# Optimization experiments

Measured on AMD Instinct MI355X. Metric: run time of the kernel, lower is better.

The kernel has to match this reference:

```python
import jax, jax.numpy as jnp
import numpy as np

N_NODES = 50000
E_RAW = 1600000
EMB_DIM = 32
HID = 128
OUT = 128


def setup_inputs() -> dict:
    key = jax.random.key(0)
    k1, k2, k3, k4, k5, k6 = jax.random.split(key, 6)
    x = jnp.arange(N_NODES, dtype=jnp.int64)
    edge_index = jax.random.randint(k1, (2, E_RAW), 0, N_NODES, dtype=jnp.int64)
    emb = jax.random.normal(k2, (N_NODES, EMB_DIM), dtype=jnp.float32)
    W1 = jax.random.normal(k3, (EMB_DIM, HID), dtype=jnp.float32) / np.sqrt(EMB_DIM)
    b1 = jnp.zeros((HID,), dtype=jnp.float32)
    W2 = jax.random.normal(k4, (HID, OUT), dtype=jnp.float32) / np.sqrt(HID)
    b2 = jnp.zeros((OUT,), dtype=jnp.float32)
    return {"x": x, "edge_index": edge_index, "emb": emb,
            "W1": W1, "b1": b1, "W2": W2, "b2": b2}


def _gcn_norm(edge_index, num_nodes):
    # add self-loops, then symmetric normalization deg^-1/2 A_hat deg^-1/2
    loop = jnp.arange(num_nodes, dtype=edge_index.dtype)
    src = jnp.concatenate([edge_index[0], loop])
    dst = jnp.concatenate([edge_index[1], loop])
    ones = jnp.ones(src.shape[0], dtype=jnp.float32)
    deg = jax.ops.segment_sum(ones, dst, num_segments=num_nodes)
    dinv = jax.lax.rsqrt(deg)  # deg >= 1 due to self-loops
    norm = dinv[src] * dinv[dst]  # [E+N]
    return src, dst, norm


def _gcn_conv(h, src, dst, norm, W, b, num_nodes):
    h = h @ W                                  # [N, d_out] dense GEMM
    msg = h[src] * norm[:, None]               # gather + edge scale
    agg = jax.ops.segment_sum(msg, dst, num_segments=num_nodes)  # scatter-add
    return agg + b


def reference(x, edge_index, emb, W1, b1, W2, b2):
    num_nodes = emb.shape[0]
    h = emb[x]                                 # embedding lookup
    src, dst, norm = _gcn_norm(edge_index, num_nodes)
    h = _gcn_conv(h, src, dst, norm, W1, b1, num_nodes)
    h = jax.nn.relu(h)
    out = _gcn_conv(h, src, dst, norm, W2, b2, num_nodes)
    return out
```

## Files before the change

kernel.cpp:

```cpp
#include <hip/hip_runtime.h>


#define NPP   6250
#define NC    32

static inline int cdiv(int a, int b){ return (a + b - 1) / b; }

__device__ __forceinline__ unsigned short f2bf(float f){
    unsigned int u = __float_as_uint(f);
    u += 0x7fffu + ((u >> 16) & 1u);
    return (unsigned short)(u >> 16);
}
__device__ __forceinline__ float bf2f(unsigned short b){
    return __uint_as_float(((unsigned int)b) << 16);
}

__global__ void k_zero_i32(int* __restrict__ p, int n){
    int i = blockIdx.x * blockDim.x + threadIdx.x;
    if (i < n) p[i] = 0;
}

__global__ __launch_bounds__(256) void k_bucket(const int* __restrict__ src,
        const int* __restrict__ dst, int E, int* __restrict__ staged,
        int* __restrict__ gcur, int npp, int C){
    __shared__ int qcnt[8];
    __shared__ int qbase[8];
    __shared__ int qbuf[8 * 256];
    int tid = threadIdx.x;
    if (tid < 8) qcnt[tid] = 0;
    __syncthreads();
    int e0 = blockIdx.x * 1024 + tid * 4;
    if (e0 + 3 < E){
        int4 d4 = *(const int4*)(dst + e0);
        int4 s4 = *(const int4*)(src + e0);
        int dd[4] = {d4.x, d4.y, d4.z, d4.w};
        int ss[4] = {s4.x, s4.y, s4.z, s4.w};
        #pragma unroll
        for (int i = 0; i < 4; i++){
            int p = dd[i] / npp;
            int pk = ((dd[i] - p * npp) << 17) | ss[i];
            int pos = atomicAdd(&qcnt[p], 1);
            if (pos < 256) qbuf[p * 256 + pos] = pk;
            else {
                int gp = atomicAdd(&gcur[p], 1);
                staged[(size_t)p * C + gp] = pk;
            }
        }
    } else {
        for (int e = e0; e < E && e < e0 + 4; e++){
            int d = dst[e], s = src[e];
            int p = d / npp;
            int pk = ((d - p * npp) << 17) | s;
            int pos = atomicAdd(&qcnt[p], 1);
            if (pos < 256) qbuf[p * 256 + pos] = pk;
            else {
                int gp = atomicAdd(&gcur[p], 1);
                staged[(size_t)p * C + gp] = pk;
            }
        }
    }
    __syncthreads();
    if (tid < 8){
        int nq = min(qcnt[tid], 256);
        qbase[tid] = (nq > 0) ? atomicAdd(&gcur[tid], nq) : 0;
    }
    __syncthreads();
    for (int b = 0; b < 8; b++){
        int nq = min(qcnt[b], 256);
        int gb = qbase[b];
        for (int i = tid; i < nq; i += 256)
            staged[(size_t)b * C + gb + i] = qbuf[b * 256 + i];
    }
}

__global__ __launch_bounds__(256) void k_hist(const int* __restrict__ staged,
        const int* __restrict__ gcur, int C, int CH, int npp,
        unsigned short* __restrict__ H){
    __shared__ int hist[NPP];
    int part  = blockIdx.x & 7;
    int chunk = blockIdx.x >> 3;
    int tid = threadIdx.x;
    for (int i = tid; i < npp; i += 256) hist[i] = 0;
    __syncthreads();
    int pc = gcur[part];
    int e0 = chunk * CH, e1 = min(e0 + CH, pc);
    const int* sd = staged + (size_t)part * C;
    for (int e = e0 + tid; e < e1; e += 256)
        atomicAdd(&hist[(unsigned)sd[e] >> 17], 1);
    __syncthreads();
    unsigned short* Hrow = H + (size_t)(part * NC + chunk) * npp;
    for (int i = tid; i < npp; i += 256) Hrow[i] = (unsigned short)hist[i];
}

__global__ __launch_bounds__(256) void k_nodescan(unsigned short* __restrict__ H,
        int npp, int n, int* __restrict__ ecount, float* __restrict__ dinv,
        int* __restrict__ bsum){
    __shared__ int s[256];
    int t = blockIdx.x * 256 + threadIdx.x;
    int run = 0;
    if (t < 8 * npp && t < n){
        int p  = t / npp;
        int dl = t - p * npp;
        #pragma unroll
        for (int c = 0; c < NC; c++){
            size_t idx = (size_t)(p * NC + c) * npp + dl;
            int v = H[idx];
            H[idx] = (unsigned short)run;
            run += v;
        }
        ecount[t] = run;
        dinv[t] = rsqrtf((float)run + 1.0f);
    }
    s[threadIdx.x] = run;
    __syncthreads();
    for (int d = 128; d > 0; d >>= 1){
        if (threadIdx.x < d) s[threadIdx.x] += s[threadIdx.x + d];
        __syncthreads();
    }
    if (threadIdx.x == 0) bsum[blockIdx.x] = s[0];
}

__global__ __launch_bounds__(256) void k_scanBC(const int* __restrict__ ecount, int n,
        const int* __restrict__ bsum, int nb, int* __restrict__ offsets){
    __shared__ int bs[256];
    __shared__ int s[256];
    int t = threadIdx.x;
    bs[t] = (t < nb) ? bsum[t] : 0;
    __syncthreads();
    if (t == 0){
        int run = 0;
        for (int b = 0; b < nb; b++){ int v = bs[b]; bs[b] = run; run += v; }
    }
    __syncthreads();
    int i = blockIdx.x * 256 + t;
    int v = (i < n) ? ecount[i] : 0;
    s[t] = v;
    __syncthreads();
    for (int d = 1; d < 256; d <<= 1){
        int x = (t >= d) ? s[t - d] : 0;
        __syncthreads();
        s[t] += x;
        __syncthreads();
    }
    if (i < n) offsets[i] = bs[blockIdx.x] + s[t] - v;
}

__global__ __launch_bounds__(256) void k_fill3(const int* __restrict__ staged,
        const int* __restrict__ gcur, int C, int CH, int npp,
        const unsigned short* __restrict__ H, const int* __restrict__ offsets,
        int* __restrict__ csr_src){
    __shared__ int cur[NPP];
    int part  = blockIdx.x & 7;
    int chunk = blockIdx.x >> 3;
    int tid = threadIdx.x;
    const unsigned short* Hrow = H + (size_t)(part * NC + chunk) * npp;
    for (int i = tid; i < npp; i += 256) cur[i] = Hrow[i];
    __syncthreads();
    int pc = gcur[part];
    int lo = part * npp;
    int e0 = chunk * CH, e1 = min(e0 + CH, pc);
    const int* sd = staged + (size_t)part * C;
    for (int e = e0 + tid; e < e1; e += 256){
        int pk = sd[e];
        int dl = (unsigned)pk >> 17;
        int r = atomicAdd(&cur[dl], 1);
        csr_src[offsets[lo + dl] + r] = pk & 0x1FFFF;
    }
}

__global__ void k_scale(const float* __restrict__ emb, const int* __restrict__ x,
                        const float* __restrict__ dinv, unsigned short* __restrict__ es, int n){
    int idx = blockIdx.x * blockDim.x + threadIdx.x;
    if (idx >= n * 8) return;
    int i  = idx >> 3;
    int c4 = (idx & 7) * 4;
    float dv = dinv[i];
    float4 v = *(const float4*)(emb + (size_t)x[i] * 32 + c4);
    ushort4 o;
    o.x = f2bf(v.x * dv); o.y = f2bf(v.y * dv);
    o.z = f2bf(v.z * dv); o.w = f2bf(v.w * dv);
    *(ushort4*)(es + (size_t)i * 32 + c4) = o;
}

__global__ __launch_bounds__(256) void k_l1(const unsigned short* __restrict__ es,
        const int* __restrict__ offsets, const int* __restrict__ ecount,
        const int* __restrict__ csr, const float* __restrict__ dinv,
        const float* __restrict__ W1, const float* __restrict__ b1,
        unsigned short* __restrict__ hs, int n){
    __shared__ float w[32 * 128];
    __shared__ float a1t[8][32];
    for (int i = threadIdx.x; i < 32 * 128; i += 256) w[i] = W1[i];
    int g    = threadIdx.x >> 5;
    int lane = threadIdx.x & 31;
    int node = blockIdx.x * 8 + g;
    if (node < n){
        int off = offsets[node], cnt = ecount[node];
        float s0 = bf2f(es[(size_t)node * 32 + lane]);
        float s1 = 0.f;
        int e = 0;
        for (; e + 16 <= cnt; e += 16){
            int idx[16];
            #pragma unroll
            for (int i = 0; i < 16; i++) idx[i] = csr[off + e + i];
            unsigned short v[16];
            #pragma unroll
            for (int i = 0; i < 16; i++) v[i] = es[(size_t)idx[i] * 32 + lane];
            #pragma unroll
            for (int i = 0; i < 16; i += 2){
                s0 += bf2f(v[i]);
                s1 += bf2f(v[i + 1]);
            }
        }
        for (; e + 8 <= cnt; e += 8){
            int idx[8];
            #pragma unroll
            for (int i = 0; i < 8; i++) idx[i] = csr[off + e + i];
            unsigned short v[8];
            #pragma unroll
            for (int i = 0; i < 8; i++) v[i] = es[(size_t)idx[i] * 32 + lane];
            #pragma unroll
            for (int i = 0; i < 8; i += 2){
                s0 += bf2f(v[i]);
                s1 += bf2f(v[i + 1]);
            }
        }
        for (; e < cnt; e++) s0 += bf2f(es[(size_t)csr[off + e] * 32 + lane]);
        a1t[g][lane] = dinv[node] * (s0 + s1);
    }
    __syncthreads();
    if (node >= n) return;
    int c4 = lane * 4;
    float4 acc = *(const float4*)(b1 + c4);
    #pragma unroll
    for (int k4 = 0; k4 < 8; k4++){
        float4 av = *(const float4*)&a1t[g][k4 * 4];
        float4 w0 = *(const float4*)&w[(k4 * 4 + 0) * 128 + c4];
        float4 w1 = *(const float4*)&w[(k4 * 4 + 1) * 128 + c4];
        float4 w2 = *(const float4*)&w[(k4 * 4 + 2) * 128 + c4];
        float4 w3 = *(const float4*)&w[(k4 * 4 + 3) * 128 + c4];
        acc.x += av.x * w0.x + av.y * w1.x + av.z * w2.x + av.w * w3.x;
        acc.y += av.x * w0.y + av.y * w1.y + av.z * w2.y + av.w * w3.y;
        acc.z += av.x * w0.z + av.y * w1.z + av.z * w2.z + av.w * w3.z;
        acc.w += av.x * w0.w + av.y * w1.w + av.z * w2.w + av.w * w3.w;
    }
    float dv = dinv[node];
    ushort4 o;
    o.x = f2bf(dv * fmaxf(acc.x, 0.f));
    o.y = f2bf(dv * fmaxf(acc.y, 0.f));
    o.z = f2bf(dv * fmaxf(acc.z, 0.f));
    o.w = f2bf(dv * fmaxf(acc.w, 0.f));
    *(ushort4*)(hs + (size_t)node * 128 + c4) = o;
}

__global__ __launch_bounds__(256) void k_l2(const unsigned short* __restrict__ hs,
        const int* __restrict__ offsets, const int* __restrict__ ecount,
        const int* __restrict__ csr, const float* __restrict__ dinv,
        const float* __restrict__ W2, const float* __restrict__ b2,
        float* __restrict__ out, int n){
    __shared__ float a2t[32 * 128];
    int g    = threadIdx.x >> 5;
    int lane = threadIdx.x & 31;
    int c4g  = lane * 4;
    #pragma unroll
    for (int j = 0; j < 4; j++){
        int nl = g + 8 * j;
        int node = blockIdx.x * 32 + nl;
        if (node < n){
            int off = offsets[node], cnt = ecount[node];
            ushort4 sv = *(const ushort4*)(hs + (size_t)node * 128 + c4g);
            float ax0 = bf2f(sv.x), ax1 = 0.f;
            float ay0 = bf2f(sv.y), ay1 = 0.f;
            float az0 = bf2f(sv.z), az1 = 0.f;
            float aw0 = bf2f(sv.w), aw1 = 0.f;
            int e = 0;
            for (; e + 8 <= cnt; e += 8){
                int i0 = csr[off + e + 0], i1 = csr[off + e + 1];
                int i2 = csr[off + e + 2], i3 = csr[off + e + 3];
                int i4 = csr[off + e + 4], i5 = csr[off + e + 5];
                int i6 = csr[off + e + 6], i7 = csr[off + e + 7];
                ushort4 v0 = *(const ushort4*)(hs + (size_t)i0 * 128 + c4g);
                ushort4 v1 = *(const ushort4*)(hs + (size_t)i1 * 128 + c4g);
                ushort4 v2 = *(const ushort4*)(hs + (size_t)i2 * 128 + c4g);
                ushort4 v3 = *(const ushort4*)(hs + (size_t)i3 * 128 + c4g);
                ushort4 v4 = *(const ushort4*)(hs + (size_t)i4 * 128 + c4g);
                ushort4 v5 = *(const ushort4*)(hs + (size_t)i5 * 128 + c4g);
                ushort4 v6 = *(const ushort4*)(hs + (size_t)i6 * 128 + c4g);
                ushort4 v7 = *(const ushort4*)(hs + (size_t)i7 * 128 + c4g);
                ax0 += bf2f(v0.x) + bf2f(v2.x) + bf2f(v4.x) + bf2f(v6.x);
                ax1 += bf2f(v1.x) + bf2f(v3.x) + bf2f(v5.x) + bf2f(v7.x);
                ay0 += bf2f(v0.y) + bf2f(v2.y) + bf2f(v4.y) + bf2f(v6.y);
                ay1 += bf2f(v1.y) + bf2f(v3.y) + bf2f(v5.y) + bf2f(v7.y);
                az0 += bf2f(v0.z) + bf2f(v2.z) + bf2f(v4.z) + bf2f(v6.z);
                az1 += bf2f(v1.z) + bf2f(v3.z) + bf2f(v5.z) + bf2f(v7.z);
                aw0 += bf2f(v0.w) + bf2f(v2.w) + bf2f(v4.w) + bf2f(v6.w);
                aw1 += bf2f(v1.w) + bf2f(v3.w) + bf2f(v5.w) + bf2f(v7.w);
            }
            for (; e < cnt; e++){
                ushort4 v = *(const ushort4*)(hs + (size_t)csr[off + e] * 128 + c4g);
                ax0 += bf2f(v.x); ay0 += bf2f(v.y); az0 += bf2f(v.z); aw0 += bf2f(v.w);
            }
            float dv = dinv[node];
            float4 r;
            r.x = dv * (ax0 + ax1); r.y = dv * (ay0 + ay1);
            r.z = dv * (az0 + az1); r.w = dv * (aw0 + aw1);
            *(float4*)&a2t[nl * 128 + c4g] = r;
        }
    }
    __syncthreads();
    int c4 = lane * 4;
    int r0 = (threadIdx.x >> 5) * 4;
    float4 bias = *(const float4*)(b2 + c4);
    float4 acc0 = bias, acc1 = bias, acc2 = bias, acc3 = bias;
    for (int k = 0; k < 128; k += 4){
        float4 a0  = *(const float4*)&a2t[(r0 + 0) * 128 + k];
        float4 a1v = *(const float4*)&a2t[(r0 + 1) * 128 + k];
        float4 a2v = *(const float4*)&a2t[(r0 + 2) * 128 + k];
        float4 a3v = *(const float4*)&a2t[(r0 + 3) * 128 + k];
        #pragma unroll
        for (int kk = 0; kk < 4; kk++){
            float4 wv = *(const float4*)(W2 + (size_t)(k + kk) * 128 + c4);
            float b0 = (kk == 0) ? a0.x  : (kk == 1) ? a0.y  : (kk == 2) ? a0.z  : a0.w;
            float b1v= (kk == 0) ? a1v.x : (kk == 1) ? a1v.y : (kk == 2) ? a1v.z : a1v.w;
            float b2v= (kk == 0) ? a2v.x : (kk == 1) ? a2v.y : (kk == 2) ? a2v.z : a2v.w;
            float b3 = (kk == 0) ? a3v.x : (kk == 1) ? a3v.y : (kk == 2) ? a3v.z : a3v.w;
            acc0.x += b0 * wv.x; acc0.y += b0 * wv.y; acc0.z += b0 * wv.z; acc0.w += b0 * wv.w;
            acc1.x += b1v * wv.x; acc1.y += b1v * wv.y; acc1.z += b1v * wv.z; acc1.w += b1v * wv.w;
            acc2.x += b2v * wv.x; acc2.y += b2v * wv.y; acc2.z += b2v * wv.z; acc2.w += b2v * wv.w;
            acc3.x += b3 * wv.x; acc3.y += b3 * wv.y; acc3.z += b3 * wv.z; acc3.w += b3 * wv.w;
        }
    }
    int rb = blockIdx.x * 32 + r0;
    if (rb + 0 < n) *(float4*)(out + (size_t)(rb + 0) * 128 + c4) = acc0;
    if (rb + 1 < n) *(float4*)(out + (size_t)(rb + 1) * 128 + c4) = acc1;
    if (rb + 2 < n) *(float4*)(out + (size_t)(rb + 2) * 128 + c4) = acc2;
    if (rb + 3 < n) *(float4*)(out + (size_t)(rb + 3) * 128 + c4) = acc3;
}

extern "C" void kernel_launch(void* const* d_in, const int* in_sizes, int n_in,
                              void* d_out, int out_size, void* d_ws, size_t ws_size,
                              hipStream_t stream){
    const int*   x    = (const int*)d_in[0];
    const int*   ei   = (const int*)d_in[1];
    const float* emb  = (const float*)d_in[2];
    const float* W1   = (const float*)d_in[3];
    const float* b1   = (const float*)d_in[4];
    const float* W2   = (const float*)d_in[5];
    const float* b2   = (const float*)d_in[6];
    const int N = in_sizes[0];
    const int E = in_sizes[1] / 2;
    const int* srcv = ei;
    const int* dstv = ei + E;
    float* out = (float*)d_out;

    char* p = (char*)d_ws;
    auto alloc = [&](size_t bytes) -> char* {
        char* r = p; p += (bytes + 255) & ~(size_t)255; return r;
    };
    int nb = cdiv(N, 256);
    int*            ecount  = (int*)           alloc((size_t)(N + 8) * 4);
    int*            gcur    = ecount + N;
    int*            offsets = (int*)           alloc((size_t)N * 4);
    int*            bsum    = (int*)           alloc((size_t)nb * 4);
    float*          dinv    = (float*)         alloc((size_t)N * 4);
    int*            csr     = (int*)           alloc((size_t)E * 4);
    unsigned short* es      = (unsigned short*)alloc((size_t)N * 32 * 2);
    unsigned short* H       = (unsigned short*)alloc((size_t)8 * NC * NPP * 2);
    unsigned short* hs      = (unsigned short*)alloc((size_t)N * 128 * 2);
    int*            staged  = (int*)           alloc((size_t)(E + 8 * 65536) * 4);
    (void)ws_size; (void)n_in; (void)out_size;

    const int npp = cdiv(N, 8);
    const int C   = E / 8 + 65536;
    const int CH  = cdiv(C, NC);

    k_zero_i32<<<1, 64, 0, stream>>>(gcur, 8);
    k_bucket  <<<cdiv(E, 1024), 256, 0, stream>>>(srcv, dstv, E, staged, gcur, npp, C);
    k_hist    <<<8 * NC, 256, 0, stream>>>(staged, gcur, C, CH, npp, H);
    k_nodescan<<<nb, 256, 0, stream>>>(H, npp, N, ecount, dinv, bsum);
    k_scanBC  <<<nb, 256, 0, stream>>>(ecount, N, bsum, nb, offsets);
    k_fill3   <<<8 * NC, 256, 0, stream>>>(staged, gcur, C, CH, npp, H, offsets, csr);

    k_scale <<<cdiv(N * 8, 256), 256, 0, stream>>>(emb, x, dinv, es, N);
    k_l1    <<<cdiv(N, 8), 256, 0, stream>>>(es, offsets, ecount, csr, dinv, W1, b1, hs, N);

    k_l2    <<<cdiv(N, 32), 256, 0, stream>>>(hs, offsets, ecount, csr, dinv, W2, b2, out, N);
}
```

Measured before the change: 266.6 us.

## Software-pipeline layer-2 gather over two interleaved nodes per warp group

The layer-2 aggregation now handles two destination nodes at once. It software-pipelines the CSR index loads and the bf16 row gathers, prefetching the next batch of 8 indices and rows while accumulating the current batch. This raises memory-level parallelism to hide gather latency in the edge-sum loop. It also adds a launch-bounds minimum of 5 blocks, which costs extra registers for the prefetch buffers and risks spills under the tighter register cap.

```diff
diff --git a/kernel.cpp b/kernel.cpp
--- a/kernel.cpp
+++ b/kernel.cpp
@@ -13,6 +13,41 @@
 }
 __device__ __forceinline__ float bf2f(unsigned short b){
     return __uint_as_float(((unsigned int)b) << 16);
+}
+
+#define ACC8(a, v) do { \
+    a[0] += bf2f(v[0].x) + bf2f(v[2].x) + bf2f(v[4].x) + bf2f(v[6].x); \
+    a[1] += bf2f(v[1].x) + bf2f(v[3].x) + bf2f(v[5].x) + bf2f(v[7].x); \
+    a[2] += bf2f(v[0].y) + bf2f(v[2].y) + bf2f(v[4].y) + bf2f(v[6].y); \
+    a[3] += bf2f(v[1].y) + bf2f(v[3].y) + bf2f(v[5].y) + bf2f(v[7].y); \
+    a[4] += bf2f(v[0].z) + bf2f(v[2].z) + bf2f(v[4].z) + bf2f(v[6].z); \
+    a[5] += bf2f(v[1].z) + bf2f(v[3].z) + bf2f(v[5].z) + bf2f(v[7].z); \
+    a[6] += bf2f(v[0].w) + bf2f(v[2].w) + bf2f(v[4].w) + bf2f(v[6].w); \
+    a[7] += bf2f(v[1].w) + bf2f(v[3].w) + bf2f(v[5].w) + bf2f(v[7].w); \
+} while (0)
+
+__device__ __forceinline__ void drain_edges(const unsigned short* __restrict__ hsc,
+        const int* __restrict__ csr, int off, int cnt, int e, float a[8]){
+    for (; e + 8 <= cnt; e += 8){
+        int i0 = csr[off + e + 0], i1 = csr[off + e + 1];
+        int i2 = csr[off + e + 2], i3 = csr[off + e + 3];
+        int i4 = csr[off + e + 4], i5 = csr[off + e + 5];
+        int i6 = csr[off + e + 6], i7 = csr[off + e + 7];
+        ushort4 v[8];
+        v[0] = *(const ushort4*)(hsc + (size_t)i0 * 128);
+        v[1] = *(const ushort4*)(hsc + (size_t)i1 * 128);
+        v[2] = *(const ushort4*)(hsc + (size_t)i2 * 128);
+        v[3] = *(const ushort4*)(hsc + (size_t)i3 * 128);
+        v[4] = *(const ushort4*)(hsc + (size_t)i4 * 128);
+        v[5] = *(const ushort4*)(hsc + (size_t)i5 * 128);
+        v[6] = *(const ushort4*)(hsc + (size_t)i6 * 128);
+        v[7] = *(const ushort4*)(hsc + (size_t)i7 * 128);
+        ACC8(a, v);
+    }
+    for (; e < cnt; e++){
+        ushort4 v = *(const ushort4*)(hsc + (size_t)csr[off + e] * 128);
+        a[0] += bf2f(v.x); a[2] += bf2f(v.y); a[4] += bf2f(v.z); a[6] += bf2f(v.w);
+    }
 }
 
 __global__ void k_zero_i32(int* __restrict__ p, int n){
@@ -252,7 +287,7 @@
     *(ushort4*)(hs + (size_t)node * 128 + c4) = o;
 }
 
-__global__ __launch_bounds__(256) void k_l2(const unsigned short* __restrict__ hs,
+__global__ __launch_bounds__(256, 5) void k_l2(const unsigned short* __restrict__ hs,
         const int* __restrict__ offsets, const int* __restrict__ ecount,
         const int* __restrict__ csr, const float* __restrict__ dinv,
         const float* __restrict__ W2, const float* __restrict__ b2,
@@ -261,49 +296,85 @@
     int g    = threadIdx.x >> 5;
     int lane = threadIdx.x & 31;
     int c4g  = lane * 4;
+    const unsigned short* hsc = hs + c4g;
     #pragma unroll
-    for (int j = 0; j < 4; j++){
-        int nl = g + 8 * j;
-        int node = blockIdx.x * 32 + nl;
-        if (node < n){
-            int off = offsets[node], cnt = ecount[node];
-            ushort4 sv = *(const ushort4*)(hs + (size_t)node * 128 + c4g);
-            float ax0 = bf2f(sv.x), ax1 = 0.f;
-            float ay0 = bf2f(sv.y), ay1 = 0.f;
-            float az0 = bf2f(sv.z), az1 = 0.f;
-            float aw0 = bf2f(sv.w), aw1 = 0.f;
-            int e = 0;
-            for (; e + 8 <= cnt; e += 8){
-                int i0 = csr[off + e + 0], i1 = csr[off + e + 1];
-                int i2 = csr[off + e + 2], i3 = csr[off + e + 3];
-                int i4 = csr[off + e + 4], i5 = csr[off + e + 5];
-                int i6 = csr[off + e + 6], i7 = csr[off + e + 7];
-                ushort4 v0 = *(const ushort4*)(hs + (size_t)i0 * 128 + c4g);
-                ushort4 v1 = *(const ushort4*)(hs + (size_t)i1 * 128 + c4g);
-                ushort4 v2 = *(const ushort4*)(hs + (size_t)i2 * 128 + c4g);
-                ushort4 v3 = *(const ushort4*)(hs + (size_t)i3 * 128 + c4g);
-                ushort4 v4 = *(const ushort4*)(hs + (size_t)i4 * 128 + c4g);
-                ushort4 v5 = *(const ushort4*)(hs + (size_t)i5 * 128 + c4g);
-                ushort4 v6 = *(const ushort4*)(hs + (size_t)i6 * 128 + c4g);
-                ushort4 v7 = *(const ushort4*)(hs + (size_t)i7 * 128 + c4g);
-                ax0 += bf2f(v0.x) + bf2f(v2.x) + bf2f(v4.x) + bf2f(v6.x);
-                ax1 += bf2f(v1.x) + bf2f(v3.x) + bf2f(v5.x) + bf2f(v7.x);
-                ay0 += bf2f(v0.y) + bf2f(v2.y) + bf2f(v4.y) + bf2f(v6.y);
-                ay1 += bf2f(v1.y) + bf2f(v3.y) + bf2f(v5.y) + bf2f(v7.y);
-                az0 += bf2f(v0.z) + bf2f(v2.z) + bf2f(v4.z) + bf2f(v6.z);
-                az1 += bf2f(v1.z) + bf2f(v3.z) + bf2f(v5.z) + bf2f(v7.z);
-                aw0 += bf2f(v0.w) + bf2f(v2.w) + bf2f(v4.w) + bf2f(v6.w);
-                aw1 += bf2f(v1.w) + bf2f(v3.w) + bf2f(v5.w) + bf2f(v7.w);
+    for (int jp = 0; jp < 2; jp++){
+        int nlA = g + 8 * (2 * jp);
+        int nlB = g + 8 * (2 * jp + 1);
+        int nodeA = blockIdx.x * 32 + nlA;
+        int nodeB = blockIdx.x * 32 + nlB;
+        bool okA = nodeA < n, okB = nodeB < n;
+        int offA = okA ? offsets[nodeA] : 0;
+        int cntA = okA ? ecount[nodeA] : 0;
+        int offB = okB ? offsets[nodeB] : 0;
+        int cntB = okB ? ecount[nodeB] : 0;
+        float aA[8], aB[8];
+        #pragma unroll
+        for (int i = 0; i < 8; i++){ aA[i] = 0.f; aB[i] = 0.f; }
+        if (okA){
+            ushort4 sv = *(const ushort4*)(hsc + (size_t)nodeA * 128);
+            aA[0] = bf2f(sv.x); aA[2] = bf2f(sv.y);
+            aA[4] = bf2f(sv.z); aA[6] = bf2f(sv.w);
+        }
+        if (okB){
+            ushort4 sv = *(const ushort4*)(hsc + (size_t)nodeB * 128);
+            aB[0] = bf2f(sv.x); aB[2] = bf2f(sv.y);
+            aB[4] = bf2f(sv.z); aB[6] = bf2f(sv.w);
+        }
+        int NA = cntA >> 3, NB = cntB >> 3;
+        int minN = min(NA, NB);
+        int eA = 0, eB = 0;
+        if (minN > 0){
+            int iA[8], iB[8];
+            ushort4 gA[8], gB[8];
+            #pragma unroll
+            for (int i = 0; i < 8; i++) iA[i] = csr[offA + i];
+            #pragma unroll
+            for (int i = 0; i < 8; i++) iB[i] = csr[offB + i];
+            #pragma unroll
+            for (int i = 0; i < 8; i++) gA[i] = *(const ushort4*)(hsc + (size_t)iA[i] * 128);
+            #pragma unroll
+            for (int i = 0; i < 8; i++) gB[i] = *(const ushort4*)(hsc + (size_t)iB[i] * 128);
+            int pA = min(8, (NA - 1) * 8);
+            int pB = min(8, (NB - 1) * 8);
+            #pragma unroll
+            for (int i = 0; i < 8; i++) iA[i] = csr[offA + pA + i];
+            #pragma unroll
+            for (int i = 0; i < 8; i++) iB[i] = csr[offB + pB + i];
+            for (int t = 1; t < minN; t++){
+                ACC8(aA, gA);
+                #pragma unroll
+                for (int i = 0; i < 8; i++) gA[i] = *(const ushort4*)(hsc + (size_t)iA[i] * 128);
+                int qA = min((t + 1) * 8, (NA - 1) * 8);
+                #pragma unroll
+                for (int i = 0; i < 8; i++) iA[i] = csr[offA + qA + i];
+                ACC8(aB, gB);
+                #pragma unroll
+                for (int i = 0; i < 8; i++) gB[i] = *(const ushort4*)(hsc + (size_t)iB[i] * 128);
+                int qB = min((t + 1) * 8, (NB - 1) * 8);
+                #pragma unroll
+                for (int i = 0; i < 8; i++) iB[i] = csr[offB + qB + i];
             }
-            for (; e < cnt; e++){
-                ushort4 v = *(const ushort4*)(hs + (size_t)csr[off + e] * 128 + c4g);
-                ax0 += bf2f(v.x); ay0 += bf2f(v.y); az0 += bf2f(v.z); aw0 += bf2f(v.w);
-            }
-            float dv = dinv[node];
+            ACC8(aA, gA);
+            ACC8(aB, gB);
+            eA = minN * 8;
+            eB = minN * 8;
+        }
+        drain_edges(hsc, csr, offA, cntA, eA, aA);
+        drain_edges(hsc, csr, offB, cntB, eB, aB);
+        if (okA){
+            float dv = dinv[nodeA];
             float4 r;
-            r.x = dv * (ax0 + ax1); r.y = dv * (ay0 + ay1);
-            r.z = dv * (az0 + az1); r.w = dv * (aw0 + aw1);
-            *(float4*)&a2t[nl * 128 + c4g] = r;
+            r.x = dv * (aA[0] + aA[1]); r.y = dv * (aA[2] + aA[3]);
+            r.z = dv * (aA[4] + aA[5]); r.w = dv * (aA[6] + aA[7]);
+            *(float4*)&a2t[nlA * 128 + c4g] = r;
+        }
+        if (okB){
+            float dv = dinv[nodeB];
+            float4 r;
+            r.x = dv * (aB[0] + aB[1]); r.y = dv * (aB[2] + aB[3]);
+            r.z = dv * (aB[4] + aB[5]); r.w = dv * (aB[6] + aB[7]);
+            *(float4*)&a2t[nlB * 128 + c4g] = r;
         }
     }
     __syncthreads();
```

Result: slower. 287.1 us (+7.7%).
